# Optimization experiments

Measured on AMD Instinct MI355X. Metric: run time of the kernel, lower is better.

Reference implementation:

```python
import jax, jax.numpy as jnp
import numpy as np

N_NODES = 50000
N_EDGES = 800000
F_IN = 128
F_OUT = 128


def gcn_conv(x, W, b, src, tgt, w, n):
    # x: [n, F_in]; GCNConv with add_self_loops=True, improved=False (fill=1.0)
    lin = x @ W  # [n, F_out]
    deg = jax.ops.segment_sum(w, tgt, num_segments=n) + 1.0  # self-loop weight 1
    dinv = jax.lax.rsqrt(deg)
    normw = dinv[src] * w * dinv[tgt]  # [E]
    agg = jax.ops.segment_sum(lin[src] * normw[:, None], tgt, num_segments=n)
    return agg + lin * (dinv * dinv)[:, None] + b


def setup_inputs() -> dict:
    key = jax.random.key(0)
    ks = jax.random.split(key, 16)
    X = jax.random.normal(ks[0], (1, N_NODES, F_IN), jnp.float32)
    edge_index = jax.random.randint(ks[1], (2, N_EDGES), 0, N_NODES, jnp.int64)
    edge_weight = jax.random.uniform(ks[2], (N_EDGES,), jnp.float32)
    H = jax.random.normal(ks[3], (1, N_NODES, F_OUT), jnp.float32)
    s = 1.0 / np.sqrt(F_IN)
    s2 = 1.0 / np.sqrt(2 * F_OUT)
    params = {
        'W_z': jax.random.uniform(ks[4], (F_IN, F_OUT), jnp.float32, -s, s),
        'b_z': jnp.zeros((F_OUT,), jnp.float32),
        'W_r': jax.random.uniform(ks[5], (F_IN, F_OUT), jnp.float32, -s, s),
        'b_r': jnp.zeros((F_OUT,), jnp.float32),
        'W_h': jax.random.uniform(ks[6], (F_IN, F_OUT), jnp.float32, -s, s),
        'b_h': jnp.zeros((F_OUT,), jnp.float32),
        'Wl_z': jax.random.uniform(ks[7], (2 * F_OUT, F_OUT), jnp.float32, -s2, s2),
        'bl_z': jax.random.uniform(ks[8], (F_OUT,), jnp.float32, -s2, s2),
        'Wl_r': jax.random.uniform(ks[9], (2 * F_OUT, F_OUT), jnp.float32, -s2, s2),
        'bl_r': jax.random.uniform(ks[10], (F_OUT,), jnp.float32, -s2, s2),
        'Wl_h': jax.random.uniform(ks[11], (2 * F_OUT, F_OUT), jnp.float32, -s2, s2),
        'bl_h': jax.random.uniform(ks[12], (F_OUT,), jnp.float32, -s2, s2),
    }
    return dict(X=X, edge_index=edge_index, edge_weight=edge_weight, H=H, **params)


def reference(X, edge_index, edge_weight, H,
              W_z, b_z, W_r, b_r, W_h, b_h,
              Wl_z, bl_z, Wl_r, bl_r, Wl_h, bl_h):
    B, N, _ = X.shape
    n = B * N
    x = X.reshape(n, -1)
    src, tgt = edge_index[0], edge_index[1]

    cz = gcn_conv(x, W_z, b_z, src, tgt, edge_weight, n).reshape(B, N, -1)
    Z = jax.nn.sigmoid(jnp.concatenate([cz, H], axis=2) @ Wl_z + bl_z)

    cr = gcn_conv(x, W_r, b_r, src, tgt, edge_weight, n).reshape(B, N, -1)
    R = jax.nn.sigmoid(jnp.concatenate([cr, H], axis=2) @ Wl_r + bl_r)

    ch = gcn_conv(x, W_h, b_h, src, tgt, edge_weight, n).reshape(B, N, -1)
    H_tilde = jnp.tanh(jnp.concatenate([ch, H * R], axis=2) @ Wl_h + bl_h)

    return Z * H + (1.0 - Z) * H_tilde
```

## Files before the change

kernel.cpp:

```cpp
#include <hip/hip_runtime.h>
#include <hip/hip_bf16.h>

#define N_NODES 50000
#define N_EDGES 800000
#define M_PAD   50048
#define NBLK5   1564
#define CAP     96

typedef __attribute__((ext_vector_type(8))) short bf16x8_t;
typedef __attribute__((ext_vector_type(4))) float f32x4_t;
typedef __attribute__((ext_vector_type(2))) float f32x2_t;

__device__ __forceinline__ unsigned short f2bf(float f) {
    unsigned u = __float_as_uint(f);
    u += 0x7FFFu + ((u >> 16) & 1u);
    return (unsigned short)(u >> 16);
}
__device__ __forceinline__ float bf2f(unsigned short h) {
    return __uint_as_float(((unsigned)h) << 16);
}


__global__ void prep1_kernel(const float* __restrict__ Wz, const float* __restrict__ Wr,
                             const float* __restrict__ Wh,
                             const float* __restrict__ bz, const float* __restrict__ br,
                             const float* __restrict__ bh,
                             const float* __restrict__ Wlz, const float* __restrict__ Wlr,
                             const float* __restrict__ Wlh,
                             const float* __restrict__ blz, const float* __restrict__ blr,
                             const float* __restrict__ blh,
                             float* __restrict__ Pf, float* __restrict__ cg,
                             int* __restrict__ counts) {
    int tid = blockIdx.x * 256 + threadIdx.x;
    if (tid < N_NODES) counts[tid] = 0;
    if (tid < 3 * 16384) {
        int g = tid / 16384, k = (tid / 128) % 128, n = tid & 127;
        const float* W  = (g == 0) ? Wz  : (g == 1) ? Wr  : Wh;
        const float* Wl = (g == 0) ? Wlz : (g == 1) ? Wlr : Wlh;
        float acc = 0.f;
        #pragma unroll 8
        for (int j = 0; j < 128; ++j)
            acc = fmaf(W[k * 128 + j], Wl[j * 128 + n], acc);
        Pf[tid] = acc;
    } else if (tid < 3 * 16384 + 384) {
        int u = tid - 3 * 16384;
        int g = u / 128, n = u & 127;
        const float* b  = (g == 0) ? bz  : (g == 1) ? br  : bh;
        const float* Wl = (g == 0) ? Wlz : (g == 1) ? Wlr : Wlh;
        const float* bl = (g == 0) ? blz : (g == 1) ? blr : blh;
        float acc = bl[n];
        #pragma unroll 8
        for (int j = 0; j < 128; ++j)
            acc = fmaf(b[j], Wl[j * 128 + n], acc);
        cg[u] = acc;
    }
}

__global__ void wfrag2_kernel(const float* __restrict__ Pf,
                              const float* __restrict__ Wlz, const float* __restrict__ Wlr,
                              const float* __restrict__ Wlh,
                              unsigned short* __restrict__ Wf2) {
    int tid = blockIdx.x * 256 + threadIdx.x;
    if (tid >= 6 * 2048) return;
    int m = tid / 2048, t = tid % 2048;
    int nt = t / 256, ks = (t / 64) % 4, lane = t % 64;
    const float* src;
    if (m < 3) src = Pf + m * 16384;
    else       src = ((m == 3) ? Wlz : (m == 4) ? Wlr : Wlh) + 128 * 128;
    unsigned short* dst = Wf2 + m * 16384 + ((nt * 4 + ks) * 64 + lane) * 8;
    int n = nt * 16 + (lane & 15);
    int k0 = ks * 32 + 8 * (lane >> 4);
    #pragma unroll
    for (int j = 0; j < 8; ++j) dst[j] = f2bf(src[(k0 + j) * 128 + n]);
}

__global__ void place_kernel(const int* __restrict__ EI, const float* __restrict__ EW,
                             int* __restrict__ counts, int2* __restrict__ rec,
                             const float* __restrict__ Hf, unsigned short* __restrict__ Hb) {
    int i = blockIdx.x * 256 + threadIdx.x;
    if (i < N_NODES * 32) {
        float4 h = ((const float4*)Hf)[i];
        ushort4 b;
        b.x = f2bf(h.x); b.y = f2bf(h.y); b.z = f2bf(h.z); b.w = f2bf(h.w);
        ((ushort4*)Hb)[i] = b;
    }
    if (i < N_EDGES) {
        int s = EI[i];
        int t = EI[N_EDGES + i];
        int pos = atomicAdd(&counts[t], 1);
        if (pos < CAP) rec[(size_t)t * CAP + pos] = make_int2(s, __float_as_int(EW[i]));
    }
}

__global__ void degconv_kernel(const int* __restrict__ counts, const int2* __restrict__ rec,
                               const float* __restrict__ X,
                               float* __restrict__ dinv, unsigned short* __restrict__ Xb,
                               unsigned* __restrict__ Xf) {
    int tid = blockIdx.x * 256 + threadIdx.x;
    int node = tid >> 4;
    int j = tid & 15;
    if (node >= N_NODES) return;
    int c = counts[node]; c = (c < CAP) ? c : CAP;
    const int2* rb = rec + (size_t)node * CAP;
    float d = 0.f;
    for (int e = j; e < c; e += 16) d += __int_as_float(rb[e].y);
    d += __shfl_xor(d, 8, 16);
    d += __shfl_xor(d, 4, 16);
    d += __shfl_xor(d, 2, 16);
    d += __shfl_xor(d, 1, 16);
    d += 1.0f;
    float di = rsqrtf(d);
    if (j == 0) dinv[node] = di;
    float4 xa = *(const float4*)(X + (size_t)node * 128 + j * 8);
    float4 xb = *(const float4*)(X + (size_t)node * 128 + j * 8 + 4);
    float s0 = di * xa.x, s1 = di * xa.y, s2 = di * xa.z, s3 = di * xa.w;
    float s4 = di * xb.x, s5 = di * xb.y, s6 = di * xb.z, s7 = di * xb.w;
    ushort4 oa, ob;
    oa.x = f2bf(s0); oa.y = f2bf(s1); oa.z = f2bf(s2); oa.w = f2bf(s3);
    ob.x = f2bf(s4); ob.y = f2bf(s5); ob.z = f2bf(s6); ob.w = f2bf(s7);
    *(ushort4*)(Xb + (size_t)node * 128 + j * 8) = oa;
    *(ushort4*)(Xb + (size_t)node * 128 + j * 8 + 4) = ob;
    int u0 = __builtin_amdgcn_cvt_pk_fp8_f32(s0, s1, 0, false);
    u0 = __builtin_amdgcn_cvt_pk_fp8_f32(s2, s3, u0, true);
    int u1 = __builtin_amdgcn_cvt_pk_fp8_f32(s4, s5, 0, false);
    u1 = __builtin_amdgcn_cvt_pk_fp8_f32(s6, s7, u1, true);
    uint2 o;
    o.x = (unsigned)u0; o.y = (unsigned)u1;
    *(uint2*)(Xf + (size_t)node * 32 + j * 2) = o;
}


__global__ __launch_bounds__(512) void fused_kernel(const unsigned short* __restrict__ Xb,
                                                    const unsigned* __restrict__ Xf,
                                                    const unsigned short* __restrict__ Hb,
                                                    const float* __restrict__ dinv,
                                                    const int* __restrict__ counts,
                                                    const int2* __restrict__ rec,
                                                    const unsigned short* __restrict__ Wf2,
                                                    const float* __restrict__ cg,
                                                    float* __restrict__ out) {
    __shared__ unsigned short ys[32][136];
    __shared__ unsigned short hs[32][136];
    __shared__ unsigned short rls[32][136];
    int tid = threadIdx.x;
    int wave = tid >> 6, lane = tid & 63;
    int rowbase = blockIdx.x * 32;
    int rlo = lane & 15;
    int kg = 8 * (lane >> 4);
    int n0 = wave;

    {
        int r = tid >> 4, co = (tid & 15) * 8;
        int row = rowbase + r;
        bf16x8_t h;
        if (row < N_NODES) h = *(const bf16x8_t*)(Hb + (size_t)row * 128 + co);
        else {
            #pragma unroll
            for (int j = 0; j < 8; ++j) h[j] = 0;
        }
        *(bf16x8_t*)(&hs[r][co]) = h;
    }

    {
        int nl = wave * 4 + (lane >> 4);
        int half = (lane >> 3) & 1;
        int lg = lane & 7;
        int node = rowbase + nl;
        float acc[16];
        #pragma unroll
        for (int j = 0; j < 16; ++j) acc[j] = 0.f;
        if (node < N_NODES) {
            if (half == 0) {
                bf16x8_t x0 = *(const bf16x8_t*)(Xb + (size_t)node * 128 + lg * 16);
                bf16x8_t x1 = *(const bf16x8_t*)(Xb + (size_t)node * 128 + lg * 16 + 8);
                #pragma unroll
                for (int j = 0; j < 8; ++j) {
                    acc[j] = bf2f((unsigned short)x0[j]);
                    acc[8 + j] = bf2f((unsigned short)x1[j]);
                }
            }
            int c = counts[node]; c = (c < CAP) ? c : CAP;
            const int2* rb = rec + (size_t)node * CAP;
            int e = half;
            int2 r;
            uint4 xa;
            float wcur = 0.f;
            if (e < c) {
                r = rb[e];
                xa = *(const uint4*)(Xf + (size_t)r.x * 32 + lg * 4);
                wcur = __int_as_float(r.y);
                if (e + 2 < c) r = rb[e + 2];
            }
            while (e < c) {
                uint4 xn;
                float wn = 0.f;
                int en = e + 2;
                if (en < c) {
                    xn = *(const uint4*)(Xf + (size_t)r.x * 32 + lg * 4);
                    wn = __int_as_float(r.y);
                    if (en + 2 < c) r = rb[en + 2];
                }
                #pragma unroll
                for (int k = 0; k < 4; ++k) {
                    unsigned u = ((const unsigned*)&xa)[k];
                    f32x2_t lo = __builtin_amdgcn_cvt_pk_f32_fp8((int)u, false);
                    f32x2_t hi = __builtin_amdgcn_cvt_pk_f32_fp8((int)u, true);
                    acc[k * 4 + 0] = fmaf(wcur, lo[0], acc[k * 4 + 0]);
                    acc[k * 4 + 1] = fmaf(wcur, lo[1], acc[k * 4 + 1]);
                    acc[k * 4 + 2] = fmaf(wcur, hi[0], acc[k * 4 + 2]);
                    acc[k * 4 + 3] = fmaf(wcur, hi[1], acc[k * 4 + 3]);
                }
                xa = xn; wcur = wn;
                e = en;
            }
        }
        #pragma unroll
        for (int j = 0; j < 16; ++j) acc[j] += __shfl_xor(acc[j], 8, 64);
        if (half == 0) {
            float dt = (node < N_NODES) ? dinv[node] : 0.f;
            ushort4 o0, o1, o2, o3;
            o0.x = f2bf(dt * acc[0]);  o0.y = f2bf(dt * acc[1]);
            o0.z = f2bf(dt * acc[2]);  o0.w = f2bf(dt * acc[3]);
            o1.x = f2bf(dt * acc[4]);  o1.y = f2bf(dt * acc[5]);
            o1.z = f2bf(dt * acc[6]);  o1.w = f2bf(dt * acc[7]);
            o2.x = f2bf(dt * acc[8]);  o2.y = f2bf(dt * acc[9]);
            o2.z = f2bf(dt * acc[10]); o2.w = f2bf(dt * acc[11]);
            o3.x = f2bf(dt * acc[12]); o3.y = f2bf(dt * acc[13]);
            o3.z = f2bf(dt * acc[14]); o3.w = f2bf(dt * acc[15]);
            *(ushort4*)(&ys[nl][lg * 16])      = o0;
            *(ushort4*)(&ys[nl][lg * 16 + 4])  = o1;
            *(ushort4*)(&ys[nl][lg * 16 + 8])  = o2;
            *(ushort4*)(&ys[nl][lg * 16 + 12]) = o3;
        }
    }
    __syncthreads();

    const unsigned short* Az = Wf2;
    const unsigned short* Ar = Wf2 + 16384;
    const unsigned short* Ah = Wf2 + 2 * 16384;
    const unsigned short* Bz = Wf2 + 3 * 16384;
    const unsigned short* Br = Wf2 + 4 * 16384;
    const unsigned short* Bh = Wf2 + 5 * 16384;
    int col = n0 * 16 + rlo;

    {
        f32x4_t a0 = f32x4_t{0.f, 0.f, 0.f, 0.f};
        f32x4_t a1 = f32x4_t{0.f, 0.f, 0.f, 0.f};
        #pragma unroll
        for (int ks = 0; ks < 4; ++ks) {
            bf16x8_t y0 = *(const bf16x8_t*)(&ys[rlo][ks * 32 + kg]);
            bf16x8_t y1 = *(const bf16x8_t*)(&ys[16 + rlo][ks * 32 + kg]);
            bf16x8_t b = *(const bf16x8_t*)(Ar + ((n0 * 4 + ks) * 64 + lane) * 8);
            a0 = __builtin_amdgcn_mfma_f32_16x16x32_bf16(y0, b, a0, 0, 0, 0);
            a1 = __builtin_amdgcn_mfma_f32_16x16x32_bf16(y1, b, a1, 0, 0, 0);
        }
        #pragma unroll
        for (int ks = 0; ks < 4; ++ks) {
            bf16x8_t h0 = *(const bf16x8_t*)(&hs[rlo][ks * 32 + kg]);
            bf16x8_t h1 = *(const bf16x8_t*)(&hs[16 + rlo][ks * 32 + kg]);
            bf16x8_t b = *(const bf16x8_t*)(Br + ((n0 * 4 + ks) * 64 + lane) * 8);
            a0 = __builtin_amdgcn_mfma_f32_16x16x32_bf16(h0, b, a0, 0, 0, 0);
            a1 = __builtin_amdgcn_mfma_f32_16x16x32_bf16(h1, b, a1, 0, 0, 0);
        }
        float crv = cg[128 + col];
        #pragma unroll
        for (int r = 0; r < 4; ++r) {
            float p0 = a0[r] + crv;
            float p1 = a1[r] + crv;
            rls[4 * (lane >> 4) + r][col] = f2bf(1.0f / (1.0f + __expf(-p0)));
            rls[16 + 4 * (lane >> 4) + r][col] = f2bf(1.0f / (1.0f + __expf(-p1)));
        }
    }
    __syncthreads();

    {
        f32x4_t az0 = f32x4_t{0.f, 0.f, 0.f, 0.f};
        f32x4_t az1 = f32x4_t{0.f, 0.f, 0.f, 0.f};
        f32x4_t at0 = f32x4_t{0.f, 0.f, 0.f, 0.f};
        f32x4_t at1 = f32x4_t{0.f, 0.f, 0.f, 0.f};
        #pragma unroll
        for (int ks = 0; ks < 4; ++ks) {
            bf16x8_t y0 = *(const bf16x8_t*)(&ys[rlo][ks * 32 + kg]);
            bf16x8_t y1 = *(const bf16x8_t*)(&ys[16 + rlo][ks * 32 + kg]);
            bf16x8_t bz_ = *(const bf16x8_t*)(Az + ((n0 * 4 + ks) * 64 + lane) * 8);
            bf16x8_t bh_ = *(const bf16x8_t*)(Ah + ((n0 * 4 + ks) * 64 + lane) * 8);
            az0 = __builtin_amdgcn_mfma_f32_16x16x32_bf16(y0, bz_, az0, 0, 0, 0);
            az1 = __builtin_amdgcn_mfma_f32_16x16x32_bf16(y1, bz_, az1, 0, 0, 0);
            at0 = __builtin_amdgcn_mfma_f32_16x16x32_bf16(y0, bh_, at0, 0, 0, 0);
            at1 = __builtin_amdgcn_mfma_f32_16x16x32_bf16(y1, bh_, at1, 0, 0, 0);
        }
        #pragma unroll
        for (int ks = 0; ks < 4; ++ks) {
            bf16x8_t h0 = *(const bf16x8_t*)(&hs[rlo][ks * 32 + kg]);
            bf16x8_t h1 = *(const bf16x8_t*)(&hs[16 + rlo][ks * 32 + kg]);
            bf16x8_t rf0 = *(const bf16x8_t*)(&rls[rlo][ks * 32 + kg]);
            bf16x8_t rf1 = *(const bf16x8_t*)(&rls[16 + rlo][ks * 32 + kg]);
            bf16x8_t hr0, hr1;
            #pragma unroll
            for (int j = 0; j < 8; ++j) {
                hr0[j] = (short)f2bf(bf2f((unsigned short)h0[j]) * bf2f((unsigned short)rf0[j]));
                hr1[j] = (short)f2bf(bf2f((unsigned short)h1[j]) * bf2f((unsigned short)rf1[j]));
            }
            bf16x8_t bz_ = *(const bf16x8_t*)(Bz + ((n0 * 4 + ks) * 64 + lane) * 8);
            bf16x8_t bh_ = *(const bf16x8_t*)(Bh + ((n0 * 4 + ks) * 64 + lane) * 8);
            az0 = __builtin_amdgcn_mfma_f32_16x16x32_bf16(h0, bz_, az0, 0, 0, 0);
            az1 = __builtin_amdgcn_mfma_f32_16x16x32_bf16(h1, bz_, az1, 0, 0, 0);
            at0 = __builtin_amdgcn_mfma_f32_16x16x32_bf16(hr0, bh_, at0, 0, 0, 0);
            at1 = __builtin_amdgcn_mfma_f32_16x16x32_bf16(hr1, bh_, at1, 0, 0, 0);
        }
        float czv = cg[col];
        float chv = cg[256 + col];
        #pragma unroll
        for (int rt = 0; rt < 2; ++rt) {
            #pragma unroll
            for (int r = 0; r < 4; ++r) {
                int rl = rt * 16 + 4 * (lane >> 4) + r;
                int row = rowbase + rl;
                if (row < N_NODES) {
                    float pz = (rt == 0 ? az0[r] : az1[r]) + czv;
                    float z = 1.0f / (1.0f + __expf(-pz));
                    float ph = (rt == 0 ? at0[r] : at1[r]) + chv;
                    float t = __expf(-2.0f * fabsf(ph));
                    float th = (1.0f - t) / (1.0f + t);
                    th = copysignf(th, ph);
                    float h = bf2f(hs[rl][col]);
                    out[(size_t)row * 128 + col] = z * h + (1.0f - z) * th;
                }
            }
        }
    }
}


extern "C" void kernel_launch(void* const* d_in, const int* in_sizes, int n_in,
                              void* d_out, int out_size, void* d_ws, size_t ws_size,
                              hipStream_t stream) {
    const float*      X   = (const float*)d_in[0];
    const int*        EI  = (const int*)d_in[1];
    const float*      EW  = (const float*)d_in[2];
    const float*      Hf  = (const float*)d_in[3];
    const float*      Wz  = (const float*)d_in[4];
    const float*      bz  = (const float*)d_in[5];
    const float*      Wr  = (const float*)d_in[6];
    const float*      br  = (const float*)d_in[7];
    const float*      Wh  = (const float*)d_in[8];
    const float*      bh  = (const float*)d_in[9];
    const float*      Wlz = (const float*)d_in[10];
    const float*      blz = (const float*)d_in[11];
    const float*      Wlr = (const float*)d_in[12];
    const float*      blr = (const float*)d_in[13];
    const float*      Wlh = (const float*)d_in[14];
    const float*      blh = (const float*)d_in[15];
    float* out = (float*)d_out;

    char* p = (char*)d_ws;
    auto alloc = [&](size_t bytes) {
        char* r = p;
        p += (bytes + 255) & ~(size_t)255;
        return r;
    };
    int*   counts = (int*)alloc(M_PAD * 4);
    float* dinv   = (float*)alloc(M_PAD * 4);
    int2*  rec    = (int2*)alloc((size_t)N_NODES * CAP * 8);
    unsigned short* Xb  = (unsigned short*)alloc((size_t)M_PAD * 128 * 2);
    unsigned*       Xf  = (unsigned*)alloc((size_t)M_PAD * 128);
    unsigned short* Hb  = (unsigned short*)alloc((size_t)M_PAD * 128 * 2);
    float* Pf  = (float*)alloc(3 * 128 * 128 * 4);
    float* cgb = (float*)alloc(3 * 128 * 4);
    unsigned short* Wf2 = (unsigned short*)alloc(6 * 128 * 128 * 2);

    prep1_kernel<<<196, 256, 0, stream>>>(Wz, Wr, Wh, bz, br, bh,
                                          Wlz, Wlr, Wlh, blz, blr, blh,
                                          Pf, cgb, counts);
    wfrag2_kernel<<<48, 256, 0, stream>>>(Pf, Wlz, Wlr, Wlh, Wf2);
    place_kernel<<<6250, 256, 0, stream>>>(EI, EW, counts, rec, Hf, Hb);
    degconv_kernel<<<3125, 256, 0, stream>>>(counts, rec, X, dinv, Xb, Xf);
    fused_kernel<<<NBLK5, 512, 0, stream>>>(Xb, Xf, Hb, dinv, counts, rec, Wf2, cgb, out);
}
```

Before: 128.9 us.

## Move X quantization into place kernel and apply source dinv per edge in gather

X is converted to bf16 and fp8 without dinv scaling inside the edge-placement kernel, overlapping it with H conversion. The degree kernel now only computes dinv. The fused gather multiplies each edge weight by dinv[src] and the self term by dinv[node]. This takes the X read and writes off the dependent degree pass, but adds a random dinv load per edge in the gather and changes the fp8 quantization of unscaled X.

```diff
diff --git a/kernel.cpp b/kernel.cpp
--- a/kernel.cpp
+++ b/kernel.cpp
@@ -76,13 +76,21 @@
 
 __global__ void place_kernel(const int* __restrict__ EI, const float* __restrict__ EW,
                              int* __restrict__ counts, int2* __restrict__ rec,
-                             const float* __restrict__ Hf, unsigned short* __restrict__ Hb) {
+                             const float* __restrict__ X, const float* __restrict__ Hf,
+                             unsigned short* __restrict__ Hb,
+                             unsigned short* __restrict__ Xb, unsigned* __restrict__ Xf) {
     int i = blockIdx.x * 256 + threadIdx.x;
     if (i < N_NODES * 32) {
         float4 h = ((const float4*)Hf)[i];
-        ushort4 b;
+        float4 x = ((const float4*)X)[i];
+        ushort4 b, a;
         b.x = f2bf(h.x); b.y = f2bf(h.y); b.z = f2bf(h.z); b.w = f2bf(h.w);
+        a.x = f2bf(x.x); a.y = f2bf(x.y); a.z = f2bf(x.z); a.w = f2bf(x.w);
         ((ushort4*)Hb)[i] = b;
+        ((ushort4*)Xb)[i] = a;
+        int u0 = __builtin_amdgcn_cvt_pk_fp8_f32(x.x, x.y, 0, false);
+        u0 = __builtin_amdgcn_cvt_pk_fp8_f32(x.z, x.w, u0, true);
+        Xf[i] = (unsigned)u0;
     }
     if (i < N_EDGES) {
         int s = EI[i];
@@ -92,10 +100,8 @@
     }
 }
 
-__global__ void degconv_kernel(const int* __restrict__ counts, const int2* __restrict__ rec,
-                               const float* __restrict__ X,
-                               float* __restrict__ dinv, unsigned short* __restrict__ Xb,
-                               unsigned* __restrict__ Xf) {
+__global__ void degdinv_kernel(const int* __restrict__ counts, const int2* __restrict__ rec,
+                               float* __restrict__ dinv) {
     int tid = blockIdx.x * 256 + threadIdx.x;
     int node = tid >> 4;
     int j = tid & 15;
@@ -109,24 +115,7 @@
     d += __shfl_xor(d, 2, 16);
     d += __shfl_xor(d, 1, 16);
     d += 1.0f;
-    float di = rsqrtf(d);
-    if (j == 0) dinv[node] = di;
-    float4 xa = *(const float4*)(X + (size_t)node * 128 + j * 8);
-    float4 xb = *(const float4*)(X + (size_t)node * 128 + j * 8 + 4);
-    float s0 = di * xa.x, s1 = di * xa.y, s2 = di * xa.z, s3 = di * xa.w;
-    float s4 = di * xb.x, s5 = di * xb.y, s6 = di * xb.z, s7 = di * xb.w;
-    ushort4 oa, ob;
-    oa.x = f2bf(s0); oa.y = f2bf(s1); oa.z = f2bf(s2); oa.w = f2bf(s3);
-    ob.x = f2bf(s4); ob.y = f2bf(s5); ob.z = f2bf(s6); ob.w = f2bf(s7);
-    *(ushort4*)(Xb + (size_t)node * 128 + j * 8) = oa;
-    *(ushort4*)(Xb + (size_t)node * 128 + j * 8 + 4) = ob;
-    int u0 = __builtin_amdgcn_cvt_pk_fp8_f32(s0, s1, 0, false);
-    u0 = __builtin_amdgcn_cvt_pk_fp8_f32(s2, s3, u0, true);
-    int u1 = __builtin_amdgcn_cvt_pk_fp8_f32(s4, s5, 0, false);
-    u1 = __builtin_amdgcn_cvt_pk_fp8_f32(s6, s7, u1, true);
-    uint2 o;
-    o.x = (unsigned)u0; o.y = (unsigned)u1;
-    *(uint2*)(Xf + (size_t)node * 32 + j * 2) = o;
+    if (j == 0) dinv[node] = rsqrtf(d);
 }
 
 
@@ -169,14 +158,16 @@
         float acc[16];
         #pragma unroll
         for (int j = 0; j < 16; ++j) acc[j] = 0.f;
+        float dt = 0.f;
         if (node < N_NODES) {
+            dt = dinv[node];
             if (half == 0) {
                 bf16x8_t x0 = *(const bf16x8_t*)(Xb + (size_t)node * 128 + lg * 16);
                 bf16x8_t x1 = *(const bf16x8_t*)(Xb + (size_t)node * 128 + lg * 16 + 8);
                 #pragma unroll
                 for (int j = 0; j < 8; ++j) {
-                    acc[j] = bf2f((unsigned short)x0[j]);
-                    acc[8 + j] = bf2f((unsigned short)x1[j]);
+                    acc[j] = dt * bf2f((unsigned short)x0[j]);
+                    acc[8 + j] = dt * bf2f((unsigned short)x1[j]);
                 }
             }
             int c = counts[node]; c = (c < CAP) ? c : CAP;
@@ -188,7 +179,7 @@
             if (e < c) {
                 r = rb[e];
                 xa = *(const uint4*)(Xf + (size_t)r.x * 32 + lg * 4);
-                wcur = __int_as_float(r.y);
+                wcur = __int_as_float(r.y) * dinv[r.x];
                 if (e + 2 < c) r = rb[e + 2];
             }
             while (e < c) {
@@ -197,7 +188,7 @@
                 int en = e + 2;
                 if (en < c) {
                     xn = *(const uint4*)(Xf + (size_t)r.x * 32 + lg * 4);
-                    wn = __int_as_float(r.y);
+                    wn = __int_as_float(r.y) * dinv[r.x];
                     if (en + 2 < c) r = rb[en + 2];
                 }
                 #pragma unroll
@@ -217,7 +208,6 @@
         #pragma unroll
         for (int j = 0; j < 16; ++j) acc[j] += __shfl_xor(acc[j], 8, 64);
         if (half == 0) {
-            float dt = (node < N_NODES) ? dinv[node] : 0.f;
             ushort4 o0, o1, o2, o3;
             o0.x = f2bf(dt * acc[0]);  o0.y = f2bf(dt * acc[1]);
             o0.z = f2bf(dt * acc[2]);  o0.w = f2bf(dt * acc[3]);
@@ -373,7 +363,7 @@
                                           Wlz, Wlr, Wlh, blz, blr, blh,
                                           Pf, cgb, counts);
     wfrag2_kernel<<<48, 256, 0, stream>>>(Pf, Wlz, Wlr, Wlh, Wf2);
-    place_kernel<<<6250, 256, 0, stream>>>(EI, EW, counts, rec, Hf, Hb);
-    degconv_kernel<<<3125, 256, 0, stream>>>(counts, rec, X, dinv, Xb, Xf);
+    place_kernel<<<6250, 256, 0, stream>>>(EI, EW, counts, rec, X, Hf, Hb, Xb, Xf);
+    degdinv_kernel<<<3125, 256, 0, stream>>>(counts, rec, dinv);
     fused_kernel<<<NBLK5, 512, 0, stream>>>(Xb, Xf, Hb, dinv, counts, rec, Wf2, cgb, out);
 }
```

Result: slower. 135.0 us (+4.7%).
